# Kernel tuning notes

Hardware: AMD Instinct MI355X
Metric: run time of the kernel (lower is better)

The kernel has to match this reference:

```python
import jax, jax.numpy as jnp
from jax import lax
import numpy as np

B = 262144   # batch of independent series
K = 64       # forecast horizon (init k)
D_IN = 200   # Non_AR_net input dim (Linear(200,100))
H = 100      # hidden width


def setup_inputs() -> dict:
    key = jax.random.key(0)
    ks = jax.random.split(key, 10)
    f32 = jnp.float32
    x = jax.random.normal(ks[0], (B, D_IN), f32)
    last_mu = jax.random.normal(ks[1], (B,), f32)
    # last_sigma is the variance state; keep it strictly positive
    last_sigma = jax.random.uniform(ks[2], (B,), f32) + 0.5
    # MLP params (Kaiming-ish scale)
    W1 = jax.random.normal(ks[3], (D_IN, H), f32) / np.float32(np.sqrt(D_IN))
    b1 = jnp.zeros((H,), f32)
    W2 = jax.random.normal(ks[4], (H, H), f32) / np.float32(np.sqrt(H))
    b2 = jnp.zeros((H,), f32)
    W3 = jax.random.normal(ks[5], (H, K), f32) / np.float32(np.sqrt(H))
    b3 = jnp.zeros((K,), f32)
    return {
        "x": x, "last_mu": last_mu, "last_sigma": last_sigma,
        "alpha_mu": jnp.asarray(0.1, f32), "alpha_sigma": jnp.asarray(0.1, f32),
        "beta_mu": jnp.asarray(0.9, f32), "beta_sigma": jnp.asarray(0.85, f32),
        "omega_mu": jnp.asarray(0.0, f32), "omega_sigma": jnp.asarray(0.05, f32),
        "nu": jnp.asarray(5.0, f32), "norm_strength": jnp.asarray(1.0, f32),
        "W1": W1, "b1": b1, "W2": W2, "b2": b2, "W3": W3, "b3": b3,
    }


def _mlp(x, W1, b1, W2, b2, W3, b3):
    h = jax.nn.relu(x @ W1 + b1)
    h = jax.nn.relu(h @ W2 + b2)
    return h @ W3 + b3  # [B, K]


def _ar_gas(deep_preds, last_mu, last_sigma, a_mu, a_s, b_mu, b_s, o_mu, o_s, nu, ns):
    """Student-t score-driven (GAS) k-step recurrence, vectorized over batch.
    deep_preds: [B, K]; state mu, sigma2: [B]."""
    w = 1.0 + 1.0 / nu

    def step(carry, y):  # y: [B]
        mu, s2 = carry
        e = y - mu
        denom = 1.0 + e * e / (nu * s2)
        mu_new = o_mu + ns * a_mu * (w * e / denom) + b_mu * mu
        s2_new = o_s + ns * a_s * (w * e * e / denom - s2) + b_s * s2
        return (mu_new, s2_new), (mu_new, s2_new)

    (_, _), (mus, s2s) = lax.scan(step, (last_mu, last_sigma), deep_preds.T)
    return mus.T, jnp.sqrt(s2s.T)  # [B, K] each


def reference(x, last_mu, last_sigma, alpha_mu, alpha_sigma, beta_mu, beta_sigma,
              omega_mu, omega_sigma, nu, norm_strength,
              W1, b1, W2, b2, W3, b3):
    deep_preds = _mlp(x, W1, b1, W2, b2, W3, b3)            # [B, K]
    dp = lax.stop_gradient(deep_preds)                       # .detach() in torch
    mu_pred, sigma_pred = _ar_gas(dp, last_mu, last_sigma,
                                  alpha_mu, alpha_sigma, beta_mu, beta_sigma,
                                  omega_mu, omega_sigma, nu, norm_strength)
    return deep_preds * sigma_pred + mu_pred                 # [B, K]
```

## Files before the change

### kernel.cpp

```cpp
#include <hip/hip_runtime.h>
#include <hip/hip_bf16.h>

typedef short v8s __attribute__((ext_vector_type(8)));
typedef float v4f __attribute__((ext_vector_type(4)));

#define THREADS 512
#define WAVES   8
#define NTILES  8
#define BMROWS  1024
#define W1F     0
#define W2F     49
#define W3F     77
#define SLABB   95232
#define SLAB_STRIDE 264
#define SLAB_SIZE   4224
#define LDS_TOTAL   (SLABB + WAVES * SLAB_SIZE)

__device__ __forceinline__ unsigned short f2bf(float f) {
    union { __hip_bfloat16 h; unsigned short u; } c;
    c.h = __float2bfloat16(f);
    return c.u;
}
__device__ __forceinline__ unsigned pk2(float a, float b) {
    return (unsigned)f2bf(a) | ((unsigned)f2bf(b) << 16);
}
__device__ __forceinline__ v4f mfma16(v8s a, v8s b, v4f c) {
    return __builtin_amdgcn_mfma_f32_16x16x32_bf16(a, b, c, 0, 0, 0);
}
__device__ __forceinline__ v8s mkfrag(float4 a, float4 b) {
    union { unsigned u[4]; v8s s; } t;
    t.u[0] = pk2(a.x, a.y); t.u[1] = pk2(a.z, a.w);
    t.u[2] = pk2(b.x, b.y); t.u[3] = pk2(b.z, b.w);
    return t.s;
}
__device__ __forceinline__ void gload_lds16(const void* g, void* l) {
    __builtin_amdgcn_global_load_lds(
        (const __attribute__((address_space(1))) void*)g,
        (__attribute__((address_space(3))) void*)l, 16, 0, 0);
}

__global__ void prep_weights(const float* __restrict__ W1,
                             const float* __restrict__ W2,
                             const float* __restrict__ W3,
                             uint4* __restrict__ wf) {
    const int bid = blockIdx.x, l = threadIdx.x;
    const float* W; int K, N, KC, base, f;
    if (bid < 49)      { W = W1; K = 200; N = 100; KC = 7; base = W1F * 64; f = bid; }
    else if (bid < 77) { W = W2; K = 100; N = 100; KC = 4; base = W2F * 64; f = bid - 49; }
    else               { W = W3; K = 100; N = 64;  KC = 4; base = W3F * 64; f = bid - 77; }
    const int kc = f % KC;
    const int n  = (f / KC) * 16 + (l & 15);
    unsigned u[4];
    #pragma unroll
    for (int p = 0; p < 4; ++p) {
        const int k0 = kc * 32 + (l >> 4) * 8 + p * 2;
        const float a = (k0     < K && n < N) ? W[(size_t)k0 * N + n]       : 0.f;
        const float b = (k0 + 1 < K && n < N) ? W[(size_t)(k0 + 1) * N + n] : 0.f;
        u[p] = pk2(a, b);
    }
    wf[base + f * 64 + l] = make_uint4(u[0], u[1], u[2], u[3]);
}

__global__ __launch_bounds__(THREADS, 2)
void ar_gas_v23(const float* __restrict__ x,
                const float* __restrict__ last_mu,
                const float* __restrict__ last_sigma,
                const float* __restrict__ p_amu, const float* __restrict__ p_as,
                const float* __restrict__ p_bmu, const float* __restrict__ p_bs,
                const float* __restrict__ p_omu, const float* __restrict__ p_os,
                const float* __restrict__ p_nu,  const float* __restrict__ p_ns,
                const float* __restrict__ b1, const float* __restrict__ b2,
                const float* __restrict__ b3,
                const uint4* __restrict__ wf,
                float* __restrict__ out)
{
    extern __shared__ __align__(16) unsigned char L[];
    const int tid  = threadIdx.x;
    const int lane = tid & 63;
    const int wid  = tid >> 6;
    const int l15  = lane & 15;
    const int l4   = lane >> 4;
    const int blk  = blockIdx.x;

    const float anu = *p_nu,  ans = *p_ns;
    const float aMu = *p_amu, aSg = *p_as;
    const float bMu = *p_bmu, bSg = *p_bs;
    const float oMu = *p_omu, oSg = *p_os;
    const float wS  = 1.f + __builtin_amdgcn_rcpf(anu);
    const float cmu = ans * aMu * wS;
    const float cs  = ans * aSg * wS;
    const float bs2 = bSg - ans * aSg;

#define XLOADT(dst, base_row, kk)                                       \
    { int kb = (kk) * 32 + l4 * 8;                                      \
      kb = (kb + 8 <= 200) ? kb : 168;     \
      const float* p_ = x + ((base_row) + l15) * 200;                   \
      dst[kk][0] = *(const float4*)(p_ + kb);                           \
      dst[kk][1] = *(const float4*)(p_ + kb + 4); }

    const size_t gw0 = (size_t)blk * BMROWS + (size_t)wid * (16 * NTILES);

    float4 xv[7][2];
    #pragma unroll
    for (int kc = 0; kc < 7; ++kc) XLOADT(xv, gw0, kc);

    for (int s = wid; s < 93; s += WAVES)
        gload_lds16(wf + s * 64 + lane, L + s * 1024);
    __syncthreads();

    for (int i = 0; i < wid; ++i) __builtin_amdgcn_s_sleep(7);

#define FRAG_W1(f)  (*(const uint4*)(&L[(W1F + (f)) * 1024 + lane * 16]))
#define FRAG_W2(f)  (*(const uint4*)(&L[(W2F + (f)) * 1024 + lane * 16]))
#define FRAG_W3(f)  (*(const uint4*)(&L[(W3F + (f)) * 1024 + lane * 16]))

    const int sb      = SLABB + wid * SLAB_SIZE;
    const int sb_epi  = sb + (l4 * 4) * SLAB_STRIDE + l15 * 2;
    const int sb_rd   = sb + l15 * SLAB_STRIDE + l4 * 16;
    const int sb_dpw  = sb + (l4 * 4) * SLAB_STRIDE + l15 * 4;
    const int sb_gas  = sb + l15 * SLAB_STRIDE;
    const int sb_st   = sb + l4 * SLAB_STRIDE + l15 * 16;

    #pragma unroll 1
    for (int t = 0; t < NTILES; ++t) {
        const size_t gw = gw0 + t * 16;

        const float mu_init = last_mu[gw + l15];
        const float s2_init = last_sigma[gw + l15];

        v4f acc[7];
        #pragma unroll
        for (int nt = 0; nt < 7; ++nt) acc[nt] = (v4f){0.f, 0.f, 0.f, 0.f};
        #pragma unroll
        for (int kc = 0; kc < 7; ++kc) {
            uint4 bu[7];
            #pragma unroll
            for (int nt = 0; nt < 7; ++nt) bu[nt] = FRAG_W1(nt * 7 + kc);
            const v8s af = mkfrag(xv[kc][0], xv[kc][1]);
            #pragma unroll
            for (int nt = 0; nt < 7; ++nt)
                acc[nt] = mfma16(af, *(const v8s*)&bu[nt], acc[nt]);
        }

        if (t < NTILES - 1) {
            #pragma unroll
            for (int kc = 0; kc < 7; ++kc) XLOADT(xv, gw0 + (t + 1) * 16, kc);
        }

        {
            float bv[7];
            #pragma unroll
            for (int nt = 0; nt < 7; ++nt) {
                const int c = nt * 16 + l15;
                bv[nt] = (c < 100) ? b1[c] : 0.f;
            }
            #pragma unroll
            for (int nt = 0; nt < 7; ++nt)
                #pragma unroll
                for (int r = 0; r < 4; ++r) {
                    const float v = fmaxf(acc[nt][r] + bv[nt], 0.f);
                    *(unsigned short*)(&L[sb_epi + r * SLAB_STRIDE + nt * 32]) =
                        f2bf(v);
                }
        }
        if (lane < 32)
            *(uint4*)(&L[sb + (lane >> 1) * SLAB_STRIDE + 224 + (lane & 1) * 16]) =
                make_uint4(0, 0, 0, 0);

        v4f acc2[7];
        #pragma unroll
        for (int nt = 0; nt < 7; ++nt) acc2[nt] = (v4f){0.f, 0.f, 0.f, 0.f};
        #pragma unroll
        for (int kc = 0; kc < 4; ++kc) {
            uint4 bu[7];
            #pragma unroll
            for (int nt = 0; nt < 7; ++nt) bu[nt] = FRAG_W2(nt * 4 + kc);
            uint4 t0 = *(const uint4*)(&L[sb_rd + kc * 64]);
            const v8s af = *(v8s*)&t0;
            #pragma unroll
            for (int nt = 0; nt < 7; ++nt)
                acc2[nt] = mfma16(af, *(const v8s*)&bu[nt], acc2[nt]);
        }
        {
            float bv[7];
            #pragma unroll
            for (int nt = 0; nt < 7; ++nt) {
                const int c = nt * 16 + l15;
                bv[nt] = (c < 100) ? b2[c] : 0.f;
            }
            #pragma unroll
            for (int nt = 0; nt < 7; ++nt)
                #pragma unroll
                for (int r = 0; r < 4; ++r) {
                    const float v = fmaxf(acc2[nt][r] + bv[nt], 0.f);
                    *(unsigned short*)(&L[sb_epi + r * SLAB_STRIDE + nt * 32]) =
                        f2bf(v);
                }
        }

        v4f acc3[4];
        #pragma unroll
        for (int nt = 0; nt < 4; ++nt) acc3[nt] = (v4f){0.f, 0.f, 0.f, 0.f};
        #pragma unroll
        for (int kc = 0; kc < 4; ++kc) {
            uint4 bu[4];
            #pragma unroll
            for (int nt = 0; nt < 4; ++nt) bu[nt] = FRAG_W3(nt * 4 + kc);
            uint4 t0 = *(const uint4*)(&L[sb_rd + kc * 64]);
            const v8s af = *(v8s*)&t0;
            #pragma unroll
            for (int nt = 0; nt < 4; ++nt)
                acc3[nt] = mfma16(af, *(const v8s*)&bu[nt], acc3[nt]);
        }
        {
            float bv[4];
            #pragma unroll
            for (int nt = 0; nt < 4; ++nt) bv[nt] = b3[nt * 16 + l15];
            #pragma unroll
            for (int nt = 0; nt < 4; ++nt)
                #pragma unroll
                for (int r = 0; r < 4; ++r)
                    *(float*)(&L[sb_dpw + r * SLAB_STRIDE + nt * 64]) =
                        acc3[nt][r] + bv[nt];
        }

        if (lane < 16) {
            float mu = mu_init;
            float s2 = s2_init;
#define GAS_STEP(Y, O)                                                  \
            {   const float e    = (Y) - mu;                            \
                const float nus2 = anu * s2;                            \
                const float den  = fmaf(e, e, nus2);                    \
                const float r0   = __builtin_amdgcn_rcpf(den);          \
                const float p    = e * nus2 * r0;                       \
                mu = fmaf(cmu, p, fmaf(bMu, mu, oMu));                  \
                s2 = fmaf(cs, e * p, fmaf(bs2, s2, oSg));               \
                (O) = fmaf((Y), __builtin_amdgcn_sqrtf(s2), mu); }
            #pragma unroll
            for (int q = 0; q < 16; ++q) {
                float4 d = *(float4*)(&L[sb_gas + q * 16]);
                float o0, o1, o2, o3;
                GAS_STEP(d.x, o0); GAS_STEP(d.y, o1);
                GAS_STEP(d.z, o2); GAS_STEP(d.w, o3);
                *(float4*)(&L[sb_gas + q * 16]) = make_float4(o0, o1, o2, o3);
            }
#undef GAS_STEP
        }

        #pragma unroll
        for (int i = 0; i < 4; ++i) {
            float4 v = *(float4*)(&L[sb_st + i * (4 * SLAB_STRIDE)]);
            ((float4*)out)[gw * 16 + i * 64 + lane] = v;
        }
    }
#undef FRAG_W1
#undef FRAG_W2
#undef FRAG_W3
#undef XLOADT
}

extern "C" void kernel_launch(void* const* d_in, const int* in_sizes, int n_in,
                              void* d_out, int out_size, void* d_ws, size_t ws_size,
                              hipStream_t stream) {
    const float* x          = (const float*)d_in[0];
    const float* last_mu    = (const float*)d_in[1];
    const float* last_sigma = (const float*)d_in[2];
    const float* amu        = (const float*)d_in[3];
    const float* asig       = (const float*)d_in[4];
    const float* bmu        = (const float*)d_in[5];
    const float* bsig       = (const float*)d_in[6];
    const float* omu        = (const float*)d_in[7];
    const float* osig       = (const float*)d_in[8];
    const float* nu         = (const float*)d_in[9];
    const float* ns         = (const float*)d_in[10];
    const float* W1         = (const float*)d_in[11];
    const float* b1         = (const float*)d_in[12];
    const float* W2         = (const float*)d_in[13];
    const float* b2         = (const float*)d_in[14];
    const float* W3         = (const float*)d_in[15];
    const float* b3         = (const float*)d_in[16];
    float* out = (float*)d_out;

    uint4* wf = (uint4*)d_ws;
    prep_weights<<<93, 64, 0, stream>>>(W1, W2, W3, wf);

    hipFuncSetAttribute((const void*)ar_gas_v23,
                        hipFuncAttributeMaxDynamicSharedMemorySize, LDS_TOTAL);

    const int B = in_sizes[1];
    dim3 grid(B / BMROWS), block(THREADS);
    ar_gas_v23<<<grid, block, LDS_TOTAL, stream>>>(
        x, last_mu, last_sigma,
        amu, asig, bmu, bsig, omu, osig, nu, ns,
        b1, b2, b3, wf, out);
}
```

Measured before the change: 75.87 us.

## Pair consecutive tiles so the GAS recurrence runs on 32 lanes at once

Each wave's LDS slab is doubled so two consecutive 16-row tiles can be buffered. The serial GAS recurrence now runs only on odd iterations, over 32 lanes covering both tiles, instead of once per tile on 16 lanes. The output stores for both tiles are deferred to that same iteration. This halves the number of latency-bound serial recurrence phases per wave. In exchange it raises LDS use close to the per-CU limit and adds some branching and register state.

Result: slower. 77.39 us (+2.0%).

```diff
diff --git a/kernel.cpp b/kernel.cpp
--- a/kernel.cpp
+++ b/kernel.cpp
@@ -13,7 +13,8 @@
 #define W3F     77
 #define SLABB   95232
 #define SLAB_STRIDE 264
-#define SLAB_SIZE   4224
+#define REGSZ   4224
+#define SLAB_SIZE   (2 * REGSZ)
 #define LDS_TOTAL   (SLABB + WAVES * SLAB_SIZE)
 
 __device__ __forceinline__ unsigned short f2bf(float f) {
@@ -62,7 +63,7 @@
 }
 
 __global__ __launch_bounds__(THREADS, 2)
-void ar_gas_v23(const float* __restrict__ x,
+void ar_gas_v26(const float* __restrict__ x,
                 const float* __restrict__ last_mu,
                 const float* __restrict__ last_sigma,
                 const float* __restrict__ p_amu, const float* __restrict__ p_as,
@@ -115,18 +116,25 @@
 #define FRAG_W3(f)  (*(const uint4*)(&L[(W3F + (f)) * 1024 + lane * 16]))
 
     const int sb      = SLABB + wid * SLAB_SIZE;
+    const int sbB     = sb + REGSZ;
     const int sb_epi  = sb + (l4 * 4) * SLAB_STRIDE + l15 * 2;
     const int sb_rd   = sb + l15 * SLAB_STRIDE + l4 * 16;
-    const int sb_dpw  = sb + (l4 * 4) * SLAB_STRIDE + l15 * 4;
-    const int sb_gas  = sb + l15 * SLAB_STRIDE;
-    const int sb_st   = sb + l4 * SLAB_STRIDE + l15 * 16;
+    const int dp_off  = (l4 * 4) * SLAB_STRIDE + l15 * 4;
+    const int st_off  = l4 * SLAB_STRIDE + l15 * 16;
+    const int gas_base = ((lane < 16) ? sbB : sb) + l15 * SLAB_STRIDE;
+
+    float mu_i = 0.f, s2_i = 1.f;
 
     #pragma unroll 1
     for (int t = 0; t < NTILES; ++t) {
         const size_t gw = gw0 + t * 16;
-
-        const float mu_init = last_mu[gw + l15];
-        const float s2_init = last_sigma[gw + l15];
+        const bool even = ((t & 1) == 0);
+        const int  dpb  = (even ? sbB : sb) + dp_off;
+
+        if (even && lane < 32) {
+            mu_i = last_mu[gw + lane];
+            s2_i = last_sigma[gw + lane];
+        }
 
         v4f acc[7];
         #pragma unroll
@@ -220,37 +228,45 @@
             for (int nt = 0; nt < 4; ++nt)
                 #pragma unroll
                 for (int r = 0; r < 4; ++r)
-                    *(float*)(&L[sb_dpw + r * SLAB_STRIDE + nt * 64]) =
+                    *(float*)(&L[dpb + r * SLAB_STRIDE + nt * 64]) =
                         acc3[nt][r] + bv[nt];
         }
 
-        if (lane < 16) {
-            float mu = mu_init;
-            float s2 = s2_init;
+        if (!even) {
+            if (lane < 32) {
+                float mu = mu_i;
+                float s2 = s2_i;
 #define GAS_STEP(Y, O)                                                  \
-            {   const float e    = (Y) - mu;                            \
-                const float nus2 = anu * s2;                            \
-                const float den  = fmaf(e, e, nus2);                    \
-                const float r0   = __builtin_amdgcn_rcpf(den);          \
-                const float p    = e * nus2 * r0;                       \
-                mu = fmaf(cmu, p, fmaf(bMu, mu, oMu));                  \
-                s2 = fmaf(cs, e * p, fmaf(bs2, s2, oSg));               \
-                (O) = fmaf((Y), __builtin_amdgcn_sqrtf(s2), mu); }
-            #pragma unroll
-            for (int q = 0; q < 16; ++q) {
-                float4 d = *(float4*)(&L[sb_gas + q * 16]);
-                float o0, o1, o2, o3;
-                GAS_STEP(d.x, o0); GAS_STEP(d.y, o1);
-                GAS_STEP(d.z, o2); GAS_STEP(d.w, o3);
-                *(float4*)(&L[sb_gas + q * 16]) = make_float4(o0, o1, o2, o3);
-            }
+                {   const float e    = (Y) - mu;                        \
+                    const float nus2 = anu * s2;                        \
+                    const float den  = fmaf(e, e, nus2);                \
+                    const float r0   = __builtin_amdgcn_rcpf(den);      \
+                    const float p    = e * nus2 * r0;                   \
+                    mu = fmaf(cmu, p, fmaf(bMu, mu, oMu));              \
+                    s2 = fmaf(cs, e * p, fmaf(bs2, s2, oSg));           \
+                    (O) = fmaf((Y), __builtin_amdgcn_sqrtf(s2), mu); }
+                #pragma unroll
+                for (int q = 0; q < 16; ++q) {
+                    float4 d = *(float4*)(&L[gas_base + q * 16]);
+                    float o0, o1, o2, o3;
+                    GAS_STEP(d.x, o0); GAS_STEP(d.y, o1);
+                    GAS_STEP(d.z, o2); GAS_STEP(d.w, o3);
+                    *(float4*)(&L[gas_base + q * 16]) =
+                        make_float4(o0, o1, o2, o3);
+                }
 #undef GAS_STEP
-        }
-
-        #pragma unroll
-        for (int i = 0; i < 4; ++i) {
-            float4 v = *(float4*)(&L[sb_st + i * (4 * SLAB_STRIDE)]);
-            ((float4*)out)[gw * 16 + i * 64 + lane] = v;
+            }
+            const size_t gwe = gw - 16;
+            #pragma unroll
+            for (int i = 0; i < 4; ++i) {
+                float4 v = *(float4*)(&L[sbB + st_off + i * (4 * SLAB_STRIDE)]);
+                ((float4*)out)[gwe * 16 + i * 64 + lane] = v;
+            }
+            #pragma unroll
+            for (int i = 0; i < 4; ++i) {
+                float4 v = *(float4*)(&L[sb + st_off + i * (4 * SLAB_STRIDE)]);
+                ((float4*)out)[gw * 16 + i * 64 + lane] = v;
+            }
         }
     }
 #undef FRAG_W1
@@ -284,12 +300,12 @@
     uint4* wf = (uint4*)d_ws;
     prep_weights<<<93, 64, 0, stream>>>(W1, W2, W3, wf);
 
-    hipFuncSetAttribute((const void*)ar_gas_v23,
+    hipFuncSetAttribute((const void*)ar_gas_v26,
                         hipFuncAttributeMaxDynamicSharedMemorySize, LDS_TOTAL);
 
     const int B = in_sizes[1];
     dim3 grid(B / BMROWS), block(THREADS);
-    ar_gas_v23<<<grid, block, LDS_TOTAL, stream>>>(
+    ar_gas_v26<<<grid, block, LDS_TOTAL, stream>>>(
         x, last_mu, last_sigma,
         amu, asig, bmu, bsig, omu, osig, nu, ns,
         b1, b2, b3, wf, out);
```
